# Performance work log

Measured on AMD Instinct MI355X. Metric: run time of the kernel, lower is better.

## Reference

```python
import jax, jax.numpy as jnp
import numpy as np

BATCH, N_REC, D_HIDDEN = 8192, 1024, 2048
RMIN, RMAX = 0.4, 0.99

def _half_glorot(key, shape):
    # VarianceScaling(scale=1/2, fan_avg, uniform): limit = sqrt(3*scale/fan_avg)
    fan_avg = (shape[0] + shape[1]) / 2.0
    limit = np.sqrt(1.5 / fan_avg)
    return jax.random.uniform(key, shape, jnp.float32, -limit, limit)

def setup_inputs() -> dict:
    key = jax.random.key(0)
    ks = jax.random.split(key, 11)
    inputs = jax.random.normal(ks[0], (BATCH, N_REC), jnp.float32)
    state_re = jax.random.normal(ks[1], (BATCH, D_HIDDEN), jnp.float32)
    state_im = jax.random.normal(ks[2], (BATCH, D_HIDDEN), jnp.float32)
    C_re = _half_glorot(ks[3], (D_HIDDEN, N_REC))
    C_im = _half_glorot(ks[4], (D_HIDDEN, N_REC))
    B_re = _half_glorot(ks[5], (N_REC, D_HIDDEN))
    B_im = _half_glorot(ks[6], (N_REC, D_HIDDEN))
    D = jax.random.normal(ks[7], (N_REC,), jnp.float32)
    numax = float(np.log(-np.log(RMIN)))
    numin = float(np.log(-np.log(RMAX)))
    nu = jax.random.uniform(ks[8], (D_HIDDEN,), jnp.float32, numin, numax)
    theta = jax.random.uniform(ks[9], (D_HIDDEN,), jnp.float32, 0.0, 3.14 / 10)
    # gamma initialized to sqrt(1 - |lambda|^2), |lambda| = exp(-exp(nu))
    gamma = jnp.sqrt(1.0 - jnp.exp(-2.0 * jnp.exp(nu)))
    return {"inputs": inputs, "state_re": state_re, "state_im": state_im,
            "B_re": B_re, "B_im": B_im, "C_re": C_re, "C_im": C_im,
            "D": D, "nu": nu, "theta": theta, "gamma": gamma}

def reference(inputs, state_re, state_im, B_re, B_im, C_re, C_im, D, nu, theta, gamma):
    # lambda = exp(-exp(nu) + i*theta), diagonal complex recurrence
    lam = (jnp.exp(-jnp.exp(nu)) * jnp.exp(1j * theta)).astype(jnp.complex64)  # [H]
    x = (state_re + 1j * state_im).astype(jnp.complex64)  # [B,H]
    B = (B_re + 1j * B_im).astype(jnp.complex64)          # [N,H]
    C = (C_re + 1j * C_im).astype(jnp.complex64)          # [H,N]
    u_ = inputs.astype(jnp.complex64)
    new_u = gamma.astype(jnp.complex64) * (u_ @ B)        # [B,H]
    x_ = x * lam + new_u                                  # diag matmul == elementwise
    y = jnp.real(x_ @ C) + D * inputs                     # [B,N]
    return y, jnp.real(x_), jnp.imag(x_)
```

## Files before the change

### kernel.cpp

```cpp
#include <hip/hip_runtime.h>
#include <hip/hip_bf16.h>

typedef __bf16 bf16;
typedef __attribute__((ext_vector_type(8))) __bf16 bf16x8;
typedef __attribute__((ext_vector_type(4))) float floatx4;

#define BATCH 8192
#define NREC  1024
#define DHID  2048

#define GLOBAL_AS __attribute__((address_space(1)))
#define LDS_AS    __attribute__((address_space(3)))

__device__ __forceinline__ bf16 to_bf16(float f) { return (bf16)f; }

__device__ __forceinline__ void async16(const void* g, void* l) {
  __builtin_amdgcn_global_load_lds((const GLOBAL_AS unsigned int*)g,
                                   (LDS_AS unsigned int*)l, 16, 0, 0);
}

__device__ __forceinline__ bf16x8 ldsFrag(const bf16* buf, int row, int q) {
  const int s = (q ^ ((row >> 1) & 3)) * 8;
  return *reinterpret_cast<const bf16x8*>(&buf[row * 32 + s]);
}


__global__ void lam_kernel(const float* __restrict__ nu, const float* __restrict__ theta,
                           float* __restrict__ lamRe, float* __restrict__ lamIm) {
  int h = blockIdx.x * blockDim.x + threadIdx.x;
  if (h < DHID) {
    float t = expf(-expf(nu[h]));
    lamRe[h] = t * cosf(theta[h]);
    lamIm[h] = t * sinf(theta[h]);
  }
}

__global__ void convert_kernel(const float* __restrict__ src, bf16* __restrict__ dst) {
  int idx = blockIdx.x * blockDim.x + threadIdx.x;
  float4 v = reinterpret_cast<const float4*>(src)[idx];
  ushort4 pk;
  pk.x = __builtin_bit_cast(unsigned short, to_bf16(v.x));
  pk.y = __builtin_bit_cast(unsigned short, to_bf16(v.y));
  pk.z = __builtin_bit_cast(unsigned short, to_bf16(v.z));
  pk.w = __builtin_bit_cast(unsigned short, to_bf16(v.w));
  *reinterpret_cast<ushort4*>(dst + (size_t)idx * 4) = pk;
}

__global__ void transpose_kernel(const float* __restrict__ src, int C,
                                 bf16* __restrict__ dst, int dstStride, float scale) {
  __shared__ float tile[32][33];
  int c0 = blockIdx.x * 32, r0 = blockIdx.y * 32;
  #pragma unroll
  for (int i = 0; i < 32; i += 8) {
    tile[threadIdx.y + i][threadIdx.x] =
        src[(size_t)(r0 + threadIdx.y + i) * C + c0 + threadIdx.x];
  }
  __syncthreads();
  #pragma unroll
  for (int i = 0; i < 32; i += 8) {
    int c = c0 + threadIdx.y + i;
    dst[(size_t)c * dstStride + r0 + threadIdx.x] =
        to_bf16(scale * tile[threadIdx.x][threadIdx.y + i]);
  }
}


__global__ __launch_bounds__(256, 2) void gemm1_kernel(
    const bf16* __restrict__ A,
    const bf16* __restrict__ BreT,
    const bf16* __restrict__ BimT,
    const float* __restrict__ state_re,
    const float* __restrict__ state_im,
    const float* __restrict__ gamma,
    const float* __restrict__ lamRe,
    const float* __restrict__ lamIm,
    float* __restrict__ xre_out,
    float* __restrict__ xim_out,
    bf16* __restrict__ Xcat)
{
  __shared__ __align__(16) bf16 Alds[2][128 * 32];
  __shared__ __align__(16) bf16 BreLds[2][128 * 32];
  __shared__ __align__(16) bf16 BimLds[2][128 * 32];

  const int tid   = threadIdx.x;
  const int mBase = blockIdx.y * 128;
  const int hBase = blockIdx.x * 128;
  const int lane  = tid & 63;
  const int wave  = tid >> 6;
  const int wr    = (wave >> 1) * 64;
  const int wc    = (wave & 1) * 64;
  const int m16   = lane & 15;
  const int q     = lane >> 4;

  floatx4 zero = {0.f, 0.f, 0.f, 0.f};
  floatx4 accRe[4][4], accIm[4][4];
  #pragma unroll
  for (int i = 0; i < 4; ++i)
    #pragma unroll
    for (int j = 0; j < 4; ++j) { accRe[i][j] = zero; accIm[i][j] = zero; }

  const int row0 = tid >> 2;
  const int wbase = wave * 512;

  auto stage = [&](int buf, int kt) {
    #pragma unroll
    for (int p = 0; p < 2; ++p) {
      const int r  = row0 + p * 64;
      const int ss = ((tid & 3) ^ ((r >> 1) & 3)) * 8;
      const size_t aoff = (size_t)(mBase + r) * 1024 + kt + ss;
      const size_t boff = (size_t)(hBase + r) * 1024 + kt + ss;
      async16(&A[aoff],    &Alds[buf][p * 2048 + wbase]);
      async16(&BreT[boff], &BreLds[buf][p * 2048 + wbase]);
      async16(&BimT[boff], &BimLds[buf][p * 2048 + wbase]);
    }
  };

  auto computeTile = [&](int buf) {
    bf16x8 aF[4], brF[4], biF[4];
    #pragma unroll
    for (int i = 0; i < 4; ++i)
      aF[i] = ldsFrag(Alds[buf], wr + i * 16 + m16, q);
    #pragma unroll
    for (int j = 0; j < 4; ++j) {
      brF[j] = ldsFrag(BreLds[buf], wc + j * 16 + m16, q);
      biF[j] = ldsFrag(BimLds[buf], wc + j * 16 + m16, q);
    }
    #pragma unroll
    for (int i = 0; i < 4; ++i)
      #pragma unroll
      for (int j = 0; j < 4; ++j) {
        accRe[i][j] = __builtin_amdgcn_mfma_f32_16x16x32_bf16(aF[i], brF[j], accRe[i][j], 0, 0, 0);
        accIm[i][j] = __builtin_amdgcn_mfma_f32_16x16x32_bf16(aF[i], biF[j], accIm[i][j], 0, 0, 0);
      }
  };

  stage(0, 0);
  __syncthreads();
  int cur = 0;
  for (int kt = 32; kt < 1024; kt += 32) {
    stage(cur ^ 1, kt);
    computeTile(cur);
    __syncthreads();
    cur ^= 1;
  }
  computeTile(cur);

  #pragma unroll
  for (int j = 0; j < 4; ++j) {
    const int h  = hBase + wc + j * 16 + m16;
    const float g  = gamma[h];
    const float lr = lamRe[h];
    const float li = lamIm[h];
    #pragma unroll
    for (int i = 0; i < 4; ++i) {
      #pragma unroll
      for (int r = 0; r < 4; ++r) {
        const int row = mBase + wr + i * 16 + q * 4 + r;
        const size_t off = (size_t)row * DHID + h;
        const float ur = g * accRe[i][j][r];
        const float ui = g * accIm[i][j][r];
        const float sr = state_re[off];
        const float si = state_im[off];
        const float xr = sr * lr - si * li + ur;
        const float xi = sr * li + si * lr + ui;
        xre_out[off] = xr;
        xim_out[off] = xi;
        const size_t xoff = (size_t)row * (2 * DHID) + h;
        Xcat[xoff]        = to_bf16(xr);
        Xcat[xoff + DHID] = to_bf16(xi);
      }
    }
  }
}


__global__ __launch_bounds__(256, 2) void gemm2_kernel(
    const bf16* __restrict__ Xcat,
    const bf16* __restrict__ CcatT,
    const float* __restrict__ Dvec,
    const float* __restrict__ inputs,
    float* __restrict__ y)
{
  __shared__ __align__(16) bf16 Alds[2][128 * 32];
  __shared__ __align__(16) bf16 Blds[2][128 * 32];

  const int tid   = threadIdx.x;
  const int mBase = blockIdx.y * 128;
  const int nBase = blockIdx.x * 128;
  const int lane  = tid & 63;
  const int wave  = tid >> 6;
  const int wr    = (wave >> 1) * 64;
  const int wc    = (wave & 1) * 64;
  const int m16   = lane & 15;
  const int q     = lane >> 4;

  floatx4 zero = {0.f, 0.f, 0.f, 0.f};
  floatx4 acc[4][4];
  #pragma unroll
  for (int i = 0; i < 4; ++i)
    #pragma unroll
    for (int j = 0; j < 4; ++j) acc[i][j] = zero;

  const int row0 = tid >> 2;
  const int wbase = wave * 512;

  auto stage = [&](int buf, int kt) {
    #pragma unroll
    for (int p = 0; p < 2; ++p) {
      const int r  = row0 + p * 64;
      const int ss = ((tid & 3) ^ ((r >> 1) & 3)) * 8;
      const size_t aoff = (size_t)(mBase + r) * 4096 + kt + ss;
      const size_t boff = (size_t)(nBase + r) * 4096 + kt + ss;
      async16(&Xcat[aoff],  &Alds[buf][p * 2048 + wbase]);
      async16(&CcatT[boff], &Blds[buf][p * 2048 + wbase]);
    }
  };

  auto computeTile = [&](int buf) {
    bf16x8 aF[4], bF[4];
    #pragma unroll
    for (int i = 0; i < 4; ++i)
      aF[i] = ldsFrag(Alds[buf], wr + i * 16 + m16, q);
    #pragma unroll
    for (int j = 0; j < 4; ++j)
      bF[j] = ldsFrag(Blds[buf], wc + j * 16 + m16, q);
    #pragma unroll
    for (int i = 0; i < 4; ++i)
      #pragma unroll
      for (int j = 0; j < 4; ++j)
        acc[i][j] = __builtin_amdgcn_mfma_f32_16x16x32_bf16(aF[i], bF[j], acc[i][j], 0, 0, 0);
  };

  stage(0, 0);
  __syncthreads();
  int cur = 0;
  for (int kt = 32; kt < 4096; kt += 32) {
    stage(cur ^ 1, kt);
    computeTile(cur);
    __syncthreads();
    cur ^= 1;
  }
  computeTile(cur);

  #pragma unroll
  for (int j = 0; j < 4; ++j) {
    const int n = nBase + wc + j * 16 + m16;
    const float dv = Dvec[n];
    #pragma unroll
    for (int i = 0; i < 4; ++i) {
      #pragma unroll
      for (int r = 0; r < 4; ++r) {
        const int row = mBase + wr + i * 16 + q * 4 + r;
        const size_t idx = (size_t)row * NREC + n;
        y[idx] = acc[i][j][r] + dv * inputs[idx];
      }
    }
  }
}


extern "C" void kernel_launch(void* const* d_in, const int* in_sizes, int n_in,
                              void* d_out, int out_size, void* d_ws, size_t ws_size,
                              hipStream_t stream) {
  (void)in_sizes; (void)n_in; (void)out_size; (void)ws_size;

  const float* inputs   = (const float*)d_in[0];
  const float* state_re = (const float*)d_in[1];
  const float* state_im = (const float*)d_in[2];
  const float* B_re     = (const float*)d_in[3];
  const float* B_im     = (const float*)d_in[4];
  const float* C_re     = (const float*)d_in[5];
  const float* C_im     = (const float*)d_in[6];
  const float* Dvec     = (const float*)d_in[7];
  const float* nu       = (const float*)d_in[8];
  const float* theta    = (const float*)d_in[9];
  const float* gamma    = (const float*)d_in[10];

  float* out     = (float*)d_out;
  float* y_out   = out;
  float* xre_out = out + (size_t)BATCH * NREC;
  float* xim_out = xre_out + (size_t)BATCH * DHID;

  char* ws = (char*)d_ws;
  bf16*  A1    = (bf16*)(ws + 0);
  bf16*  BreT  = (bf16*)(ws + 16777216);
  bf16*  BimT  = (bf16*)(ws + 20971520);
  bf16*  CcatT = (bf16*)(ws + 25165824);
  bf16*  Xcat  = (bf16*)(ws + 33554432);
  float* lamRe = (float*)(ws + 100663296);
  float* lamIm = (float*)(ws + 100671488);

  lam_kernel<<<dim3(DHID / 256), dim3(256), 0, stream>>>(nu, theta, lamRe, lamIm);
  convert_kernel<<<dim3((BATCH * NREC) / 1024), dim3(256), 0, stream>>>(inputs, A1);

  dim3 tb(32, 8);
  transpose_kernel<<<dim3(2048 / 32, 1024 / 32), tb, 0, stream>>>(B_re, 2048, BreT, 1024, 1.0f);
  transpose_kernel<<<dim3(2048 / 32, 1024 / 32), tb, 0, stream>>>(B_im, 2048, BimT, 1024, 1.0f);
  transpose_kernel<<<dim3(1024 / 32, 2048 / 32), tb, 0, stream>>>(C_re, 1024, CcatT, 4096, 1.0f);
  transpose_kernel<<<dim3(1024 / 32, 2048 / 32), tb, 0, stream>>>(C_im, 1024, CcatT + 2048, 4096, -1.0f);

  gemm1_kernel<<<dim3(DHID / 128, BATCH / 128), dim3(256), 0, stream>>>(
      A1, BreT, BimT, state_re, state_im, gamma, lamRe, lamIm, xre_out, xim_out, Xcat);

  gemm2_kernel<<<dim3(NREC / 128, BATCH / 128), dim3(256), 0, stream>>>(
      Xcat, CcatT, Dvec, inputs, y_out);
}
```

Measured before the change: 638.6 us.

## Use 8 waves per block in both GEMMs with smaller per-wave tiles

Both GEMM kernels move from 256 to 512 threads per 128x128 block. Each wave now computes a 64x32 sub-tile instead of 64x64, and each thread issues one async load per matrix per stage instead of two. The aim is fewer accumulator registers per thread and more resident waves to hide latency. In exchange each wave reuses less data from LDS (A fragments are read by twice as many waves), and the higher launch-bounds occupancy targets may limit registers.

Measured after the change: 565.6 us. 11.4% less time.

```diff
diff --git a/kernel.cpp b/kernel.cpp
--- a/kernel.cpp
+++ b/kernel.cpp
@@ -65,7 +65,7 @@
 }
 
 
-__global__ __launch_bounds__(256, 2) void gemm1_kernel(
+__global__ __launch_bounds__(512, 3) void gemm1_kernel(
     const bf16* __restrict__ A,
     const bf16* __restrict__ BreT,
     const bf16* __restrict__ BimT,
@@ -87,48 +87,44 @@
   const int hBase = blockIdx.x * 128;
   const int lane  = tid & 63;
   const int wave  = tid >> 6;
-  const int wr    = (wave >> 1) * 64;
-  const int wc    = (wave & 1) * 64;
+  const int wr    = (wave >> 2) * 64;
+  const int wc    = (wave & 3) * 32;
   const int m16   = lane & 15;
   const int q     = lane >> 4;
 
   floatx4 zero = {0.f, 0.f, 0.f, 0.f};
-  floatx4 accRe[4][4], accIm[4][4];
+  floatx4 accRe[4][2], accIm[4][2];
   #pragma unroll
   for (int i = 0; i < 4; ++i)
     #pragma unroll
-    for (int j = 0; j < 4; ++j) { accRe[i][j] = zero; accIm[i][j] = zero; }
+    for (int j = 0; j < 2; ++j) { accRe[i][j] = zero; accIm[i][j] = zero; }
 
   const int row0 = tid >> 2;
+  const int ss   = ((tid & 3) ^ ((row0 >> 1) & 3)) * 8;
   const int wbase = wave * 512;
 
   auto stage = [&](int buf, int kt) {
-    #pragma unroll
-    for (int p = 0; p < 2; ++p) {
-      const int r  = row0 + p * 64;
-      const int ss = ((tid & 3) ^ ((r >> 1) & 3)) * 8;
-      const size_t aoff = (size_t)(mBase + r) * 1024 + kt + ss;
-      const size_t boff = (size_t)(hBase + r) * 1024 + kt + ss;
-      async16(&A[aoff],    &Alds[buf][p * 2048 + wbase]);
-      async16(&BreT[boff], &BreLds[buf][p * 2048 + wbase]);
-      async16(&BimT[boff], &BimLds[buf][p * 2048 + wbase]);
-    }
+    const size_t aoff = (size_t)(mBase + row0) * 1024 + kt + ss;
+    const size_t boff = (size_t)(hBase + row0) * 1024 + kt + ss;
+    async16(&A[aoff],    &Alds[buf][wbase]);
+    async16(&BreT[boff], &BreLds[buf][wbase]);
+    async16(&BimT[boff], &BimLds[buf][wbase]);
   };
 
   auto computeTile = [&](int buf) {
-    bf16x8 aF[4], brF[4], biF[4];
+    bf16x8 aF[4], brF[2], biF[2];
     #pragma unroll
     for (int i = 0; i < 4; ++i)
       aF[i] = ldsFrag(Alds[buf], wr + i * 16 + m16, q);
     #pragma unroll
-    for (int j = 0; j < 4; ++j) {
+    for (int j = 0; j < 2; ++j) {
       brF[j] = ldsFrag(BreLds[buf], wc + j * 16 + m16, q);
       biF[j] = ldsFrag(BimLds[buf], wc + j * 16 + m16, q);
     }
     #pragma unroll
     for (int i = 0; i < 4; ++i)
       #pragma unroll
-      for (int j = 0; j < 4; ++j) {
+      for (int j = 0; j < 2; ++j) {
         accRe[i][j] = __builtin_amdgcn_mfma_f32_16x16x32_bf16(aF[i], brF[j], accRe[i][j], 0, 0, 0);
         accIm[i][j] = __builtin_amdgcn_mfma_f32_16x16x32_bf16(aF[i], biF[j], accIm[i][j], 0, 0, 0);
       }
@@ -146,7 +142,7 @@
   computeTile(cur);
 
   #pragma unroll
-  for (int j = 0; j < 4; ++j) {
+  for (int j = 0; j < 2; ++j) {
     const int h  = hBase + wc + j * 16 + m16;
     const float g  = gamma[h];
     const float lr = lamRe[h];
@@ -174,7 +170,7 @@
 }
 
 
-__global__ __launch_bounds__(256, 2) void gemm2_kernel(
+__global__ __launch_bounds__(512, 4) void gemm2_kernel(
     const bf16* __restrict__ Xcat,
     const bf16* __restrict__ CcatT,
     const float* __restrict__ Dvec,
@@ -189,45 +185,41 @@
   const int nBase = blockIdx.x * 128;
   const int lane  = tid & 63;
   const int wave  = tid >> 6;
-  const int wr    = (wave >> 1) * 64;
-  const int wc    = (wave & 1) * 64;
+  const int wr    = (wave >> 2) * 64;
+  const int wc    = (wave & 3) * 32;
   const int m16   = lane & 15;
   const int q     = lane >> 4;
 
   floatx4 zero = {0.f, 0.f, 0.f, 0.f};
-  floatx4 acc[4][4];
+  floatx4 acc[4][2];
   #pragma unroll
   for (int i = 0; i < 4; ++i)
     #pragma unroll
-    for (int j = 0; j < 4; ++j) acc[i][j] = zero;
+    for (int j = 0; j < 2; ++j) acc[i][j] = zero;
 
   const int row0 = tid >> 2;
+  const int ss   = ((tid & 3) ^ ((row0 >> 1) & 3)) * 8;
   const int wbase = wave * 512;
 
   auto stage = [&](int buf, int kt) {
-    #pragma unroll
-    for (int p = 0; p < 2; ++p) {
-      const int r  = row0 + p * 64;
-      const int ss = ((tid & 3) ^ ((r >> 1) & 3)) * 8;
-      const size_t aoff = (size_t)(mBase + r) * 4096 + kt + ss;
-      const size_t boff = (size_t)(nBase + r) * 4096 + kt + ss;
-      async16(&Xcat[aoff],  &Alds[buf][p * 2048 + wbase]);
-      async16(&CcatT[boff], &Blds[buf][p * 2048 + wbase]);
-    }
+    const size_t aoff = (size_t)(mBase + row0) * 4096 + kt + ss;
+    const size_t boff = (size_t)(nBase + row0) * 4096 + kt + ss;
+    async16(&Xcat[aoff],  &Alds[buf][wbase]);
+    async16(&CcatT[boff], &Blds[buf][wbase]);
   };
 
   auto computeTile = [&](int buf) {
-    bf16x8 aF[4], bF[4];
+    bf16x8 aF[4], bF[2];
     #pragma unroll
     for (int i = 0; i < 4; ++i)
       aF[i] = ldsFrag(Alds[buf], wr + i * 16 + m16, q);
     #pragma unroll
-    for (int j = 0; j < 4; ++j)
+    for (int j = 0; j < 2; ++j)
       bF[j] = ldsFrag(Blds[buf], wc + j * 16 + m16, q);
     #pragma unroll
     for (int i = 0; i < 4; ++i)
       #pragma unroll
-      for (int j = 0; j < 4; ++j)
+      for (int j = 0; j < 2; ++j)
         acc[i][j] = __builtin_amdgcn_mfma_f32_16x16x32_bf16(aF[i], bF[j], acc[i][j], 0, 0, 0);
   };
 
@@ -243,7 +235,7 @@
   computeTile(cur);
 
   #pragma unroll
-  for (int j = 0; j < 4; ++j) {
+  for (int j = 0; j < 2; ++j) {
     const int n = nBase + wc + j * 16 + m16;
     const float dv = Dvec[n];
     #pragma unroll
@@ -299,9 +291,9 @@
   transpose_kernel<<<dim3(1024 / 32, 2048 / 32), tb, 0, stream>>>(C_re, 1024, CcatT, 4096, 1.0f);
   transpose_kernel<<<dim3(1024 / 32, 2048 / 32), tb, 0, stream>>>(C_im, 1024, CcatT + 2048, 4096, -1.0f);
 
-  gemm1_kernel<<<dim3(DHID / 128, BATCH / 128), dim3(256), 0, stream>>>(
+  gemm1_kernel<<<dim3(DHID / 128, BATCH / 128), dim3(512), 0, stream>>>(
       A1, BreT, BimT, state_re, state_im, gamma, lamRe, lamIm, xre_out, xim_out, Xcat);
 
-  gemm2_kernel<<<dim3(NREC / 128, BATCH / 128), dim3(256), 0, stream>>>(
+  gemm2_kernel<<<dim3(NREC / 128, BATCH / 128), dim3(512), 0, stream>>>(
       Xcat, CcatT, Dvec, inputs, y_out);
 }
```
